# Kernel optimization log

Hardware: AMD Instinct MI355X
Metric: run time of the kernel (lower is better)

## Reference

```python
import jax, jax.numpy as jnp
import numpy as np

N = 50000      # nodes
E = 800000     # edges
IN_DIM = 256
HID = 96
OUT = 64
K = 2
ALPHA = 0.15
SCALING = 1.8  # NormalizedGCNConv scaling_factor
EPS = 1e-12    # torch F.normalize eps


def setup_inputs() -> dict:
    key = jax.random.key(0)
    ks = jax.random.split(key, 8)
    x = jax.random.normal(ks[0], (N, IN_DIM), jnp.float32)
    edge_index = jax.random.randint(ks[1], (2, E), 0, N, dtype=jnp.int64)
    def lin(k, fi, fo):
        s = 1.0 / np.sqrt(fi)
        kw, kb = jax.random.split(k)
        W = jax.random.uniform(kw, (fi, fo), jnp.float32, -s, s)
        b = jax.random.uniform(kb, (fo,), jnp.float32, -s, s)
        return W, b
    W0, b0 = lin(ks[2], IN_DIM, HID)   # convs[0]
    W1, b1 = lin(ks[3], HID, HID)      # convs[1]
    Wx, bx = lin(ks[4], HID, OUT)      # convx
    return {"x": x, "edge_index": edge_index,
            "W0": W0, "b0": b0, "W1": W1, "b1": b1, "Wx": Wx, "bx": bx}


def _l2norm(x):
    n = jnp.linalg.norm(x, axis=1, keepdims=True)
    return x / jnp.maximum(n, EPS)


def _gcn_norm(edge_index):
    # add self loops, symmetric normalization D^-1/2 (A+I) D^-1/2
    loop = jnp.arange(N, dtype=edge_index.dtype)
    row = jnp.concatenate([edge_index[0], loop])
    col = jnp.concatenate([edge_index[1], loop])
    deg = jax.ops.segment_sum(jnp.ones(row.shape[0], jnp.float32), col, num_segments=N)
    dinv = jnp.where(deg > 0, jax.lax.rsqrt(jnp.maximum(deg, 1.0)), 0.0)
    norm = dinv[row] * dinv[col]   # [E+N]
    return row, col, norm


def _norm_gcn_conv(x, W, b, row, col, norm):
    # linear -> L2 normalize * 1.8 -> APPNP(K, alpha), eval mode (no dropout)
    x = x @ W + b
    x = _l2norm(x) * SCALING
    h = x
    for _ in range(K):
        agg = jax.ops.segment_sum(x[row] * norm[:, None], col, num_segments=N)
        x = (1.0 - ALPHA) * agg + ALPHA * h
    return x


def reference(x, edge_index, W0, b0, W1, b1, Wx, bx):
    row, col, norm = _gcn_norm(edge_index)
    out = jax.nn.relu(_norm_gcn_conv(x, W0, b0, row, col, norm))
    # depth=3, link_len=2: loop runs i=1 only, residual condition never fires
    out = _l2norm(_norm_gcn_conv(out, W1, b1, row, col, norm)) * 1.5
    return _norm_gcn_conv(out, Wx, bx, row, col, norm)
```

## Files before the change

kernel.cpp:

```cpp
#include <hip/hip_runtime.h>
#include <hip/hip_fp16.h>
#include <math.h>

#define BETA_C 0.85f
#define ALF_C  0.15f
#define SLOTS 48

typedef _Float16 f16x8 __attribute__((ext_vector_type(8)));
typedef float f32x4 __attribute__((ext_vector_type(4)));

__device__ inline f16x8 as_h8(uint4 v) { union { uint4 u; f16x8 h; } U; U.u = v; return U.h; }

__global__ __launch_bounds__(256) void k_fill_tlp(
        const int* __restrict__ row, const int* __restrict__ col,
        int* __restrict__ cur, int* __restrict__ adj, int E, unsigned mulc) {
    int cls = blockIdx.x & 7;
    int e = (blockIdx.x >> 3) * 256 + threadIdx.x;
    if (e >= E) return;
    int c = col[e];
    if ((int)(((unsigned long long)(unsigned)c * mulc) >> 32) != cls) return;
    int p = atomicAdd(&cur[c], 1);
    if (p < SLOTS) adj[(size_t)c * SLOTS + p] = row[e];
}

__global__ void k_prep(const int* __restrict__ cur, float2* __restrict__ dinv2,
                       int* __restrict__ adj, int n, int t0,
                       const float* __restrict__ W0, const float* __restrict__ W1,
                       const float* __restrict__ Wx, ushort* __restrict__ WT0,
                       ushort* __restrict__ WT1, ushort* __restrict__ WTx) {
    int idx = blockIdx.x * blockDim.x + threadIdx.x;
    if (idx < n) {
        int deg = cur[idx];
        float degf = (float)deg + 1.0f;
        dinv2[idx] = make_float2(rsqrtf(degf), ALF_C * sqrtf(degf));
        int ds = min(deg, SLOTS);
        int d4 = (ds + 3) & ~3;
        int* ap = adj + (size_t)idx * SLOTS;
        for (int p = ds; p < d4; ++p) ap[p] = idx;
    } else if (idx >= t0) {
        const int S0 = 96 * 256, S1 = 96 * 96, S2 = 64 * 96;
        int li = idx - t0;
        const float* W; ushort* WT; int FI, FO;
        if (li < S0)           { W = W0; WT = WT0; FI = 256; FO = 96; }
        else if (li < S0 + S1) { W = W1; WT = WT1; FI = 96;  FO = 96; li -= S0; }
        else if (li < S0+S1+S2){ W = Wx; WT = WTx; FI = 96;  FO = 64; li -= S0 + S1; }
        else return;
        int nrow = li / FI, k = li % FI;
        _Float16 hv = (_Float16)W[(size_t)k * FO + nrow];
        WT[li] = *(ushort*)&hv;
    }
}

template<int FI, int FO, int ASRC_F16>
__global__ __launch_bounds__(256) void k_gemm_mfma(
        const void* __restrict__ Xv, const ushort* __restrict__ WT,
        const float* __restrict__ Bias, const float2* __restrict__ dinv2,
        ushort* __restrict__ H, int n, float scale) {
    constexpr int NT = FO / 16;
    constexpr int CPR = FI / 8;
    __shared__ ushort sA[64 * FI];
    __shared__ ushort sW[FO * FI];
    const int tid = threadIdx.x;
    const int rb = blockIdx.x * 64;

    {
        constexpr int TOT = FO * CPR;
#pragma unroll
        for (int idx = tid; idx < TOT; idx += 256) {
            int nrow = idx / CPR, c = idx % CPR;
            uint4 v = *(((const uint4*)WT) + (size_t)nrow * CPR + c);
            int byte = ((nrow * FI + c * 8) * 2) ^ ((nrow & 7) << 4);
            *(uint4*)((char*)sW + byte) = v;
        }
    }
    {
        constexpr int TOT = 64 * CPR;
#pragma unroll
        for (int idx = tid; idx < TOT; idx += 256) {
            int r = idx / CPR, c = idx % CPR;
            int gr = rb + r;
            uint4 v = make_uint4(0u, 0u, 0u, 0u);
            if (ASRC_F16) {
                if (gr < n) v = *(((const uint4*)Xv) + (size_t)gr * CPR + c);
            } else {
                if (gr < n) {
                    const float4* Xp = (const float4*)Xv;
                    float4 f0 = Xp[(size_t)gr * (FI / 4) + c * 2];
                    float4 f1 = Xp[(size_t)gr * (FI / 4) + c * 2 + 1];
                    _Float16 hv[8] = {(_Float16)f0.x, (_Float16)f0.y, (_Float16)f0.z,
                                      (_Float16)f0.w, (_Float16)f1.x, (_Float16)f1.y,
                                      (_Float16)f1.z, (_Float16)f1.w};
                    v = *(uint4*)hv;
                }
            }
            int byte = ((r * FI + c * 8) * 2) ^ ((r & 7) << 4);
            *(uint4*)((char*)sA + byte) = v;
        }
    }
    __syncthreads();

    const int lane = tid & 63;
    const int wave = tid >> 6;
    const int lcol = lane & 15;
    const int lk = lane >> 4;

    f32x4 acc[NT];
#pragma unroll
    for (int t = 0; t < NT; ++t) acc[t] = (f32x4){0.f, 0.f, 0.f, 0.f};

    const int arow = wave * 16 + lcol;
    char* sAb = (char*)sA;
    char* sWb = (char*)sW;
#pragma unroll
    for (int s = 0; s < FI / 32; ++s) {
        int abyte = ((arow * FI + s * 32 + lk * 8) * 2) ^ ((arow & 7) << 4);
        f16x8 af = *(f16x8*)(sAb + abyte);
#pragma unroll
        for (int t = 0; t < NT; ++t) {
            int nrow = t * 16 + lcol;
            int bbyte = ((nrow * FI + s * 32 + lk * 8) * 2) ^ ((nrow & 7) << 4);
            f16x8 bf = *(f16x8*)(sWb + bbyte);
            acc[t] = __builtin_amdgcn_mfma_f32_16x16x32_f16(af, bf, acc[t], 0, 0, 0);
        }
    }

    float bv[NT];
#pragma unroll
    for (int t = 0; t < NT; ++t) bv[t] = Bias[t * 16 + lcol];
    float ss[4] = {0.f, 0.f, 0.f, 0.f};
#pragma unroll
    for (int t = 0; t < NT; ++t)
#pragma unroll
        for (int r = 0; r < 4; ++r) {
            acc[t][r] += bv[t];
            ss[r] += acc[t][r] * acc[t][r];
        }
    for (int m = 1; m < 16; m <<= 1) {
#pragma unroll
        for (int r = 0; r < 4; ++r) ss[r] += __shfl_xor(ss[r], m, 64);
    }
#pragma unroll
    for (int r = 0; r < 4; ++r) {
        int grow = rb + wave * 16 + lk * 4 + r;
        if (grow < n) {
            float sc = scale * dinv2[grow].x / fmaxf(sqrtf(ss[r]), 1e-12f);
#pragma unroll
            for (int t = 0; t < NT; ++t) {
                _Float16 hv = (_Float16)(acc[t][r] * sc);
                H[(size_t)grow * FO + t * 16 + lcol] = *(ushort*)&hv;
            }
        }
    }
}

__device__ inline void unpack8(uint4 v, float* f) {
    union { uint4 u; _Float16 h[8]; } U; U.u = v;
#pragma unroll
    for (int i = 0; i < 8; ++i) f[i] = (float)U.h[i];
}

template<int C8>
__device__ inline void gather_h(const uint4* __restrict__ tab,
                                const int* __restrict__ ap,
                                int d4, int j, f16x8& A0, f16x8& A1) {
    const int4* ap4 = (const int4*)ap;
    int e = 0;
    for (; e + 8 <= d4; e += 8) {
        int4 a0 = ap4[e >> 2];
        int4 a1 = ap4[(e >> 2) + 1];
        uint4 v0 = tab[(size_t)(unsigned)a0.x * C8 + j];
        uint4 v1 = tab[(size_t)(unsigned)a0.y * C8 + j];
        uint4 v2 = tab[(size_t)(unsigned)a0.z * C8 + j];
        uint4 v3 = tab[(size_t)(unsigned)a0.w * C8 + j];
        uint4 v4 = tab[(size_t)(unsigned)a1.x * C8 + j];
        uint4 v5 = tab[(size_t)(unsigned)a1.y * C8 + j];
        uint4 v6 = tab[(size_t)(unsigned)a1.z * C8 + j];
        uint4 v7 = tab[(size_t)(unsigned)a1.w * C8 + j];
        A0 += (as_h8(v0) + as_h8(v1)) + (as_h8(v2) + as_h8(v3));
        A1 += (as_h8(v4) + as_h8(v5)) + (as_h8(v6) + as_h8(v7));
    }
    if (e < d4) {
        int4 a0 = ap4[e >> 2];
        uint4 v0 = tab[(size_t)(unsigned)a0.x * C8 + j];
        uint4 v1 = tab[(size_t)(unsigned)a0.y * C8 + j];
        uint4 v2 = tab[(size_t)(unsigned)a0.z * C8 + j];
        uint4 v3 = tab[(size_t)(unsigned)a0.w * C8 + j];
        A0 += as_h8(v0) + as_h8(v1);
        A1 += as_h8(v2) + as_h8(v3);
    }
}

template<int C8, int TPB>
__global__ __launch_bounds__(TPB) void k_prop1(
        const uint4* __restrict__ y0, uint4* __restrict__ y1,
        const int* __restrict__ adj, const int* __restrict__ cnt,
        const float2* __restrict__ dinv2, int n) {
    int tid = threadIdx.x;
    int j = tid % C8, cl = tid / C8;
    int c = blockIdx.x * (TPB / C8) + cl;
    if (c >= n) return;
    uint4 sv = y0[(size_t)c * C8 + j];
    float d = dinv2[c].x;
    float a = BETA_C * d * d;
    int deg = min(cnt[c], SLOTS);
    int d4 = (deg + 3) & ~3;
    float coef_s = (a + ALF_C) - a * (float)(d4 - deg);
    f16x8 A0 = {0, 0, 0, 0, 0, 0, 0, 0};
    f16x8 A1 = {0, 0, 0, 0, 0, 0, 0, 0};
    gather_h<C8>(y0, adj + (size_t)c * SLOTS, d4, j, A0, A1);
    float sf[8];
    unpack8(sv, sf);
    _Float16 hv[8];
#pragma unroll
    for (int i = 0; i < 8; ++i) {
        float acc = (float)A0[i] + (float)A1[i];
        hv[i] = (_Float16)(a * acc + coef_s * sf[i]);
    }
    y1[(size_t)c * C8 + j] = *(uint4*)hv;
}

template<int C8, int TPB, int ACT, int OUTF32, int NORM>
__global__ __launch_bounds__(TPB) void k_prop2(
        const uint4* __restrict__ y1, const uint4* __restrict__ y0,
        void* __restrict__ out, const int* __restrict__ adj,
        const int* __restrict__ cnt, const float2* __restrict__ dinv2,
        int n, float nscale) {
    __shared__ float ssh[NORM ? TPB : 1];
    int tid = threadIdx.x;
    int j = tid % C8, cl = tid / C8;
    int c = blockIdx.x * (TPB / C8) + cl;
    if (!NORM && c >= n) return;
    bool on = !NORM || c < n;
    float res[8] = {0, 0, 0, 0, 0, 0, 0, 0};
    if (on) {
        uint4 sv1 = y1[(size_t)c * C8 + j];
        uint4 sv0 = y0[(size_t)c * C8 + j];
        float2 dv = dinv2[c];
        float a = BETA_C * dv.x;
        float t = dv.y;
        int deg = min(cnt[c], SLOTS);
        int d4 = (deg + 3) & ~3;
        float coef_s = a * (1.0f - (float)(d4 - deg));
        f16x8 A0 = {0, 0, 0, 0, 0, 0, 0, 0};
        f16x8 A1 = {0, 0, 0, 0, 0, 0, 0, 0};
        gather_h<C8>(y1, adj + (size_t)c * SLOTS, d4, j, A0, A1);
        float sf[8], tf[8];
        unpack8(sv1, sf);
        unpack8(sv0, tf);
#pragma unroll
        for (int i = 0; i < 8; ++i) {
            float acc = (float)A0[i] + (float)A1[i];
            res[i] = a * acc + coef_s * sf[i] + t * tf[i];
            if (ACT) res[i] = fmaxf(res[i], 0.f);
        }
    }
    if (NORM) {
        float part = 0.f;
#pragma unroll
        for (int i = 0; i < 8; ++i) part += res[i] * res[i];
        ssh[tid] = part;
        __syncthreads();
        if (!on) return;
        float tot = 0.f;
#pragma unroll
        for (int q = 0; q < C8; ++q) tot += ssh[cl * C8 + q];
        float sc = nscale / fmaxf(sqrtf(tot), 1e-12f);
        _Float16 hv[8];
#pragma unroll
        for (int i = 0; i < 8; ++i) hv[i] = (_Float16)(res[i] * sc);
        ((uint4*)out)[(size_t)c * C8 + j] = *(uint4*)hv;
    } else if (OUTF32) {
        float4* op = (float4*)out;
        op[(size_t)c * (C8 * 2) + j * 2]     = make_float4(res[0], res[1], res[2], res[3]);
        op[(size_t)c * (C8 * 2) + j * 2 + 1] = make_float4(res[4], res[5], res[6], res[7]);
    } else {
        _Float16 hv[8];
#pragma unroll
        for (int i = 0; i < 8; ++i) hv[i] = (_Float16)res[i];
        ((uint4*)out)[(size_t)c * C8 + j] = *(uint4*)hv;
    }
}

extern "C" void kernel_launch(void* const* d_in, const int* in_sizes, int n_in,
                              void* d_out, int out_size, void* d_ws, size_t ws_size,
                              hipStream_t stream) {
    const float* x  = (const float*)d_in[0];
    const int*   ei = (const int*)d_in[1];
    const float* W0 = (const float*)d_in[2];
    const float* b0 = (const float*)d_in[3];
    const float* W1 = (const float*)d_in[4];
    const float* b1 = (const float*)d_in[5];
    const float* Wx = (const float*)d_in[6];
    const float* bx = (const float*)d_in[7];
    float* out = (float*)d_out;

    const int N = in_sizes[0] / 256;
    const int E = in_sizes[1] / 2;
    const int* row = ei;
    const int* col = ei + E;

    char* ws = (char*)d_ws;
    size_t off = 0;
    auto alloc = [&](size_t bytes) -> char* {
        char* p = ws + off;
        off += (bytes + 255) & ~(size_t)255;
        return p;
    };
    int*    cur   = (int*)alloc((size_t)N * 4);
    float2* dinv2 = (float2*)alloc((size_t)N * 8);
    int*    adj   = (int*)alloc((size_t)N * SLOTS * 4);
    ushort* WT0   = (ushort*)alloc((size_t)96 * 256 * 2);
    ushort* WT1   = (ushort*)alloc((size_t)96 * 96 * 2);
    ushort* WTx   = (ushort*)alloc((size_t)64 * 96 * 2);
    ushort* Hh    = (ushort*)alloc((size_t)N * 96 * 2);
    ushort* T1h   = (ushort*)alloc((size_t)N * 96 * 2);
    ushort* T2h   = (ushort*)alloc((size_t)N * 96 * 2);
    (void)ws_size; (void)n_in; (void)out_size;

    unsigned mulc = (unsigned)((((unsigned long long)8 << 32) + (unsigned)N - 1) / (unsigned)N);

    hipMemsetAsync(cur, 0, (size_t)N * 4, stream);
    {
        int chunks = (E + 255) / 256;
        k_fill_tlp<<<chunks * 8, 256, 0, stream>>>(row, col, cur, adj, E, mulc);
    }
    {
        int t0 = ((N + 255) / 256) * 256;
        int tot = t0 + 96 * 256 + 96 * 96 + 64 * 96;
        k_prep<<<(tot + 255) / 256, 256, 0, stream>>>(cur, dinv2, adj, N, t0,
                                                      W0, W1, Wx, WT0, WT1, WTx);
    }

    int gblk = (N + 63) / 64;
    int gp12 = (N + 15) / 16;
    int gp8  = (N + 31) / 32;

    k_gemm_mfma<256, 96, 0><<<gblk, 256, 0, stream>>>(x, WT0, b0, dinv2, Hh, N, 1.8f);
    k_prop1<12, 192><<<gp12, 192, 0, stream>>>(
        (const uint4*)Hh, (uint4*)T1h, adj, cur, dinv2, N);
    k_prop2<12, 192, 1, 0, 0><<<gp12, 192, 0, stream>>>(
        (const uint4*)T1h, (const uint4*)Hh, T2h, adj, cur, dinv2, N, 0.f);

    k_gemm_mfma<96, 96, 1><<<gblk, 256, 0, stream>>>(T2h, WT1, b1, dinv2, Hh, N, 1.8f);
    k_prop1<12, 192><<<gp12, 192, 0, stream>>>(
        (const uint4*)Hh, (uint4*)T1h, adj, cur, dinv2, N);
    k_prop2<12, 192, 0, 0, 1><<<gp12, 192, 0, stream>>>(
        (const uint4*)T1h, (const uint4*)Hh, T2h, adj, cur, dinv2, N, 1.5f);

    k_gemm_mfma<96, 64, 1><<<gblk, 256, 0, stream>>>(T2h, WTx, bx, dinv2, Hh, N, 1.8f);
    k_prop1<8, 256><<<gp8, 256, 0, stream>>>(
        (const uint4*)Hh, (uint4*)T1h, adj, cur, dinv2, N);
    k_prop2<8, 256, 0, 1, 0><<<gp8, 256, 0, stream>>>(
        (const uint4*)T1h, (const uint4*)Hh, out, adj, cur, dinv2, N, 0.f);
}
```

Measured before the change: 219.1 us.

## Gather neighbor features from FP8 shadow copies in first two conv layers

The GEMM and prop1 kernels now also write a scaled FP8 copy of their outputs. The first two layers' propagation kernels gather neighbor rows from that FP8 copy instead of FP16, which halves the bytes moved per random gather, and accumulate in fp32. The cost is extra FP8 stores and conversion work, plus lower precision in the aggregated messages that may push accuracy close to tolerance. The adjacency and edge-index loads are also marked nontemporal.

```diff
diff --git a/kernel.cpp b/kernel.cpp
--- a/kernel.cpp
+++ b/kernel.cpp
@@ -5,11 +5,37 @@
 #define BETA_C 0.85f
 #define ALF_C  0.15f
 #define SLOTS 48
+#define SCALE_Q 16.0f
+#define INV_SQ  0.0625f
 
 typedef _Float16 f16x8 __attribute__((ext_vector_type(8)));
 typedef float f32x4 __attribute__((ext_vector_type(4)));
+typedef float f32x2 __attribute__((ext_vector_type(2)));
+typedef int i32x4 __attribute__((ext_vector_type(4)));
 
 __device__ inline f16x8 as_h8(uint4 v) { union { uint4 u; f16x8 h; } U; U.u = v; return U.h; }
+
+__device__ inline void unpack8(uint4 v, float* f) {
+    union { uint4 u; _Float16 h[8]; } U; U.u = v;
+#pragma unroll
+    for (int i = 0; i < 8; ++i) f[i] = (float)U.h[i];
+}
+
+__device__ inline void acc_q(uint2 q, float* acc) {
+    f32x2 f0 = __builtin_amdgcn_cvt_pk_f32_fp8((int)q.x, false);
+    f32x2 f1 = __builtin_amdgcn_cvt_pk_f32_fp8((int)q.x, true);
+    f32x2 f2 = __builtin_amdgcn_cvt_pk_f32_fp8((int)q.y, false);
+    f32x2 f3 = __builtin_amdgcn_cvt_pk_f32_fp8((int)q.y, true);
+    acc[0] += f0.x; acc[1] += f0.y; acc[2] += f1.x; acc[3] += f1.y;
+    acc[4] += f2.x; acc[5] += f2.y; acc[6] += f3.x; acc[7] += f3.y;
+}
+__device__ inline uint2 pack_q(const float* r) {
+    int lo = __builtin_amdgcn_cvt_pk_fp8_f32(r[0] * SCALE_Q, r[1] * SCALE_Q, 0, false);
+    lo = __builtin_amdgcn_cvt_pk_fp8_f32(r[2] * SCALE_Q, r[3] * SCALE_Q, lo, true);
+    int hi = __builtin_amdgcn_cvt_pk_fp8_f32(r[4] * SCALE_Q, r[5] * SCALE_Q, 0, false);
+    hi = __builtin_amdgcn_cvt_pk_fp8_f32(r[6] * SCALE_Q, r[7] * SCALE_Q, hi, true);
+    return make_uint2((unsigned)lo, (unsigned)hi);
+}
 
 __global__ __launch_bounds__(256) void k_fill_tlp(
         const int* __restrict__ row, const int* __restrict__ col,
@@ -17,10 +43,11 @@
     int cls = blockIdx.x & 7;
     int e = (blockIdx.x >> 3) * 256 + threadIdx.x;
     if (e >= E) return;
-    int c = col[e];
+    int c = __builtin_nontemporal_load(col + e);
     if ((int)(((unsigned long long)(unsigned)c * mulc) >> 32) != cls) return;
+    int r = __builtin_nontemporal_load(row + e);
     int p = atomicAdd(&cur[c], 1);
-    if (p < SLOTS) adj[(size_t)c * SLOTS + p] = row[e];
+    if (p < SLOTS) adj[(size_t)c * SLOTS + p] = r;
 }
 
 __global__ void k_prep(const int* __restrict__ cur, float2* __restrict__ dinv2,
@@ -51,11 +78,12 @@
     }
 }
 
-template<int FI, int FO, int ASRC_F16>
+template<int FI, int FO, int ASRC_F16, int WQ>
 __global__ __launch_bounds__(256) void k_gemm_mfma(
         const void* __restrict__ Xv, const ushort* __restrict__ WT,
         const float* __restrict__ Bias, const float2* __restrict__ dinv2,
-        ushort* __restrict__ H, int n, float scale) {
+        ushort* __restrict__ H, unsigned char* __restrict__ Hq,
+        int n, float scale) {
     constexpr int NT = FO / 16;
     constexpr int CPR = FI / 8;
     __shared__ ushort sA[64 * FI];
@@ -146,85 +174,127 @@
             float sc = scale * dinv2[grow].x / fmaxf(sqrtf(ss[r]), 1e-12f);
 #pragma unroll
             for (int t = 0; t < NT; ++t) {
-                _Float16 hv = (_Float16)(acc[t][r] * sc);
+                float v = acc[t][r] * sc;
+                _Float16 hv = (_Float16)v;
                 H[(size_t)grow * FO + t * 16 + lcol] = *(ushort*)&hv;
+                if (WQ) {
+                    float vs = v * SCALE_Q;
+                    int b = __builtin_amdgcn_cvt_pk_fp8_f32(vs, vs, 0, false);
+                    Hq[(size_t)grow * FO + t * 16 + lcol] = (unsigned char)(b & 0xff);
+                }
             }
         }
     }
 }
 
-__device__ inline void unpack8(uint4 v, float* f) {
-    union { uint4 u; _Float16 h[8]; } U; U.u = v;
-#pragma unroll
-    for (int i = 0; i < 8; ++i) f[i] = (float)U.h[i];
+template<int C8>
+__device__ inline void gather_q(const unsigned char* __restrict__ tq,
+                                const int* __restrict__ ap,
+                                int d4, int j, float* acc) {
+    const size_t RB = C8 * 8;
+    const int jb = j * 8;
+    int e = 0;
+    for (; e + 8 <= d4; e += 8) {
+        i32x4 a0 = __builtin_nontemporal_load((const i32x4*)ap + (e >> 2));
+        i32x4 a1 = __builtin_nontemporal_load((const i32x4*)ap + (e >> 2) + 1);
+        uint2 q0 = *(const uint2*)(tq + (size_t)(unsigned)a0[0] * RB + jb);
+        uint2 q1 = *(const uint2*)(tq + (size_t)(unsigned)a0[1] * RB + jb);
+        uint2 q2 = *(const uint2*)(tq + (size_t)(unsigned)a0[2] * RB + jb);
+        uint2 q3 = *(const uint2*)(tq + (size_t)(unsigned)a0[3] * RB + jb);
+        uint2 q4 = *(const uint2*)(tq + (size_t)(unsigned)a1[0] * RB + jb);
+        uint2 q5 = *(const uint2*)(tq + (size_t)(unsigned)a1[1] * RB + jb);
+        uint2 q6 = *(const uint2*)(tq + (size_t)(unsigned)a1[2] * RB + jb);
+        uint2 q7 = *(const uint2*)(tq + (size_t)(unsigned)a1[3] * RB + jb);
+        acc_q(q0, acc); acc_q(q1, acc); acc_q(q2, acc); acc_q(q3, acc);
+        acc_q(q4, acc); acc_q(q5, acc); acc_q(q6, acc); acc_q(q7, acc);
+    }
+    if (e < d4) {
+        i32x4 a0 = __builtin_nontemporal_load((const i32x4*)ap + (e >> 2));
+        uint2 q0 = *(const uint2*)(tq + (size_t)(unsigned)a0[0] * RB + jb);
+        uint2 q1 = *(const uint2*)(tq + (size_t)(unsigned)a0[1] * RB + jb);
+        uint2 q2 = *(const uint2*)(tq + (size_t)(unsigned)a0[2] * RB + jb);
+        uint2 q3 = *(const uint2*)(tq + (size_t)(unsigned)a0[3] * RB + jb);
+        acc_q(q0, acc); acc_q(q1, acc); acc_q(q2, acc); acc_q(q3, acc);
+    }
 }
 
 template<int C8>
 __device__ inline void gather_h(const uint4* __restrict__ tab,
                                 const int* __restrict__ ap,
                                 int d4, int j, f16x8& A0, f16x8& A1) {
-    const int4* ap4 = (const int4*)ap;
     int e = 0;
     for (; e + 8 <= d4; e += 8) {
-        int4 a0 = ap4[e >> 2];
-        int4 a1 = ap4[(e >> 2) + 1];
-        uint4 v0 = tab[(size_t)(unsigned)a0.x * C8 + j];
-        uint4 v1 = tab[(size_t)(unsigned)a0.y * C8 + j];
-        uint4 v2 = tab[(size_t)(unsigned)a0.z * C8 + j];
-        uint4 v3 = tab[(size_t)(unsigned)a0.w * C8 + j];
-        uint4 v4 = tab[(size_t)(unsigned)a1.x * C8 + j];
-        uint4 v5 = tab[(size_t)(unsigned)a1.y * C8 + j];
-        uint4 v6 = tab[(size_t)(unsigned)a1.z * C8 + j];
-        uint4 v7 = tab[(size_t)(unsigned)a1.w * C8 + j];
+        i32x4 a0 = __builtin_nontemporal_load((const i32x4*)ap + (e >> 2));
+        i32x4 a1 = __builtin_nontemporal_load((const i32x4*)ap + (e >> 2) + 1);
+        uint4 v0 = tab[(size_t)(unsigned)a0[0] * C8 + j];
+        uint4 v1 = tab[(size_t)(unsigned)a0[1] * C8 + j];
+        uint4 v2 = tab[(size_t)(unsigned)a0[2] * C8 + j];
+        uint4 v3 = tab[(size_t)(unsigned)a0[3] * C8 + j];
+        uint4 v4 = tab[(size_t)(unsigned)a1[0] * C8 + j];
+        uint4 v5 = tab[(size_t)(unsigned)a1[1] * C8 + j];
+        uint4 v6 = tab[(size_t)(unsigned)a1[2] * C8 + j];
+        uint4 v7 = tab[(size_t)(unsigned)a1[3] * C8 + j];
         A0 += (as_h8(v0) + as_h8(v1)) + (as_h8(v2) + as_h8(v3));
         A1 += (as_h8(v4) + as_h8(v5)) + (as_h8(v6) + as_h8(v7));
     }
     if (e < d4) {
-        int4 a0 = ap4[e >> 2];
-        uint4 v0 = tab[(size_t)(unsigned)a0.x * C8 + j];
-        uint4 v1 = tab[(size_t)(unsigned)a0.y * C8 + j];
-        uint4 v2 = tab[(size_t)(unsigned)a0.z * C8 + j];
-        uint4 v3 = tab[(size_t)(unsigned)a0.w * C8 + j];
+        i32x4 a0 = __builtin_nontemporal_load((const i32x4*)ap + (e >> 2));
+        uint4 v0 = tab[(size_t)(unsigned)a0[0] * C8 + j];
+        uint4 v1 = tab[(size_t)(unsigned)a0[1] * C8 + j];
+        uint4 v2 = tab[(size_t)(unsigned)a0[2] * C8 + j];
+        uint4 v3 = tab[(size_t)(unsigned)a0[3] * C8 + j];
         A0 += as_h8(v0) + as_h8(v1);
         A1 += as_h8(v2) + as_h8(v3);
     }
 }
 
-template<int C8, int TPB>
+template<int C8, int TPB, int QG, int WQ>
 __global__ __launch_bounds__(TPB) void k_prop1(
-        const uint4* __restrict__ y0, uint4* __restrict__ y1,
+        const uint4* __restrict__ y0h, const unsigned char* __restrict__ y0q,
+        uint4* __restrict__ y1h, unsigned char* __restrict__ y1q,
         const int* __restrict__ adj, const int* __restrict__ cnt,
         const float2* __restrict__ dinv2, int n) {
     int tid = threadIdx.x;
     int j = tid % C8, cl = tid / C8;
     int c = blockIdx.x * (TPB / C8) + cl;
     if (c >= n) return;
-    uint4 sv = y0[(size_t)c * C8 + j];
+    uint4 sv = y0h[(size_t)c * C8 + j];
     float d = dinv2[c].x;
     float a = BETA_C * d * d;
     int deg = min(cnt[c], SLOTS);
     int d4 = (deg + 3) & ~3;
     float coef_s = (a + ALF_C) - a * (float)(d4 - deg);
-    f16x8 A0 = {0, 0, 0, 0, 0, 0, 0, 0};
-    f16x8 A1 = {0, 0, 0, 0, 0, 0, 0, 0};
-    gather_h<C8>(y0, adj + (size_t)c * SLOTS, d4, j, A0, A1);
+    float acc[8] = {0, 0, 0, 0, 0, 0, 0, 0};
+    if (QG) {
+        gather_q<C8>(y0q, adj + (size_t)c * SLOTS, d4, j, acc);
+#pragma unroll
+        for (int i = 0; i < 8; ++i) acc[i] *= INV_SQ;
+    } else {
+        f16x8 A0 = {0, 0, 0, 0, 0, 0, 0, 0};
+        f16x8 A1 = {0, 0, 0, 0, 0, 0, 0, 0};
+        gather_h<C8>(y0h, adj + (size_t)c * SLOTS, d4, j, A0, A1);
+#pragma unroll
+        for (int i = 0; i < 8; ++i) acc[i] = (float)A0[i] + (float)A1[i];
+    }
     float sf[8];
     unpack8(sv, sf);
+    float r[8];
     _Float16 hv[8];
 #pragma unroll
     for (int i = 0; i < 8; ++i) {
-        float acc = (float)A0[i] + (float)A1[i];
-        hv[i] = (_Float16)(a * acc + coef_s * sf[i]);
-    }
-    y1[(size_t)c * C8 + j] = *(uint4*)hv;
-}
-
-template<int C8, int TPB, int ACT, int OUTF32, int NORM>
+        r[i] = a * acc[i] + coef_s * sf[i];
+        hv[i] = (_Float16)r[i];
+    }
+    y1h[(size_t)c * C8 + j] = *(uint4*)hv;
+    if (WQ) *(uint2*)(y1q + (size_t)c * (C8 * 8) + j * 8) = pack_q(r);
+}
+
+template<int C8, int TPB, int ACT, int OUTF32, int NORM, int QG>
 __global__ __launch_bounds__(TPB) void k_prop2(
-        const uint4* __restrict__ y1, const uint4* __restrict__ y0,
-        void* __restrict__ out, const int* __restrict__ adj,
-        const int* __restrict__ cnt, const float2* __restrict__ dinv2,
-        int n, float nscale) {
+        const uint4* __restrict__ y1h, const unsigned char* __restrict__ y1q,
+        const uint4* __restrict__ y0h, void* __restrict__ out,
+        const int* __restrict__ adj, const int* __restrict__ cnt,
+        const float2* __restrict__ dinv2, int n, float nscale) {
     __shared__ float ssh[NORM ? TPB : 1];
     int tid = threadIdx.x;
     int j = tid % C8, cl = tid / C8;
@@ -233,24 +303,32 @@
     bool on = !NORM || c < n;
     float res[8] = {0, 0, 0, 0, 0, 0, 0, 0};
     if (on) {
-        uint4 sv1 = y1[(size_t)c * C8 + j];
-        uint4 sv0 = y0[(size_t)c * C8 + j];
+        uint4 sv1 = y1h[(size_t)c * C8 + j];
+        uint4 sv0 = y0h[(size_t)c * C8 + j];
         float2 dv = dinv2[c];
         float a = BETA_C * dv.x;
         float t = dv.y;
         int deg = min(cnt[c], SLOTS);
         int d4 = (deg + 3) & ~3;
         float coef_s = a * (1.0f - (float)(d4 - deg));
-        f16x8 A0 = {0, 0, 0, 0, 0, 0, 0, 0};
-        f16x8 A1 = {0, 0, 0, 0, 0, 0, 0, 0};
-        gather_h<C8>(y1, adj + (size_t)c * SLOTS, d4, j, A0, A1);
+        float acc[8] = {0, 0, 0, 0, 0, 0, 0, 0};
+        if (QG) {
+            gather_q<C8>(y1q, adj + (size_t)c * SLOTS, d4, j, acc);
+#pragma unroll
+            for (int i = 0; i < 8; ++i) acc[i] *= INV_SQ;
+        } else {
+            f16x8 A0 = {0, 0, 0, 0, 0, 0, 0, 0};
+            f16x8 A1 = {0, 0, 0, 0, 0, 0, 0, 0};
+            gather_h<C8>(y1h, adj + (size_t)c * SLOTS, d4, j, A0, A1);
+#pragma unroll
+            for (int i = 0; i < 8; ++i) acc[i] = (float)A0[i] + (float)A1[i];
+        }
         float sf[8], tf[8];
         unpack8(sv1, sf);
         unpack8(sv0, tf);
 #pragma unroll
         for (int i = 0; i < 8; ++i) {
-            float acc = (float)A0[i] + (float)A1[i];
-            res[i] = a * acc + coef_s * sf[i] + t * tf[i];
+            res[i] = a * acc[i] + coef_s * sf[i] + t * tf[i];
             if (ACT) res[i] = fmaxf(res[i], 0.f);
         }
     }
@@ -315,6 +393,8 @@
     ushort* Hh    = (ushort*)alloc((size_t)N * 96 * 2);
     ushort* T1h   = (ushort*)alloc((size_t)N * 96 * 2);
     ushort* T2h   = (ushort*)alloc((size_t)N * 96 * 2);
+    unsigned char* Hq  = (unsigned char*)alloc((size_t)N * 96);
+    unsigned char* T1q = (unsigned char*)alloc((size_t)N * 96);
     (void)ws_size; (void)n_in; (void)out_size;
 
     unsigned mulc = (unsigned)((((unsigned long long)8 << 32) + (unsigned)N - 1) / (unsigned)N);
@@ -335,21 +415,21 @@
     int gp12 = (N + 15) / 16;
     int gp8  = (N + 31) / 32;
 
-    k_gemm_mfma<256, 96, 0><<<gblk, 256, 0, stream>>>(x, WT0, b0, dinv2, Hh, N, 1.8f);
-    k_prop1<12, 192><<<gp12, 192, 0, stream>>>(
-        (const uint4*)Hh, (uint4*)T1h, adj, cur, dinv2, N);
-    k_prop2<12, 192, 1, 0, 0><<<gp12, 192, 0, stream>>>(
-        (const uint4*)T1h, (const uint4*)Hh, T2h, adj, cur, dinv2, N, 0.f);
-
-    k_gemm_mfma<96, 96, 1><<<gblk, 256, 0, stream>>>(T2h, WT1, b1, dinv2, Hh, N, 1.8f);
-    k_prop1<12, 192><<<gp12, 192, 0, stream>>>(
-        (const uint4*)Hh, (uint4*)T1h, adj, cur, dinv2, N);
-    k_prop2<12, 192, 0, 0, 1><<<gp12, 192, 0, stream>>>(
-        (const uint4*)T1h, (const uint4*)Hh, T2h, adj, cur, dinv2, N, 1.5f);
-
-    k_gemm_mfma<96, 64, 1><<<gblk, 256, 0, stream>>>(T2h, WTx, bx, dinv2, Hh, N, 1.8f);
-    k_prop1<8, 256><<<gp8, 256, 0, stream>>>(
-        (const uint4*)Hh, (uint4*)T1h, adj, cur, dinv2, N);
-    k_prop2<8, 256, 0, 1, 0><<<gp8, 256, 0, stream>>>(
-        (const uint4*)T1h, (const uint4*)Hh, out, adj, cur, dinv2, N, 0.f);
-}
+    k_gemm_mfma<256, 96, 0, 1><<<gblk, 256, 0, stream>>>(x, WT0, b0, dinv2, Hh, Hq, N, 1.8f);
+    k_prop1<12, 192, 1, 1><<<gp12, 192, 0, stream>>>(
+        (const uint4*)Hh, Hq, (uint4*)T1h, T1q, adj, cur, dinv2, N);
+    k_prop2<12, 192, 1, 0, 0, 1><<<gp12, 192, 0, stream>>>(
+        (const uint4*)T1h, T1q, (const uint4*)Hh, T2h, adj, cur, dinv2, N, 0.f);
+
+    k_gemm_mfma<96, 96, 1, 1><<<gblk, 256, 0, stream>>>(T2h, WT1, b1, dinv2, Hh, Hq, N, 1.8f);
+    k_prop1<12, 192, 1, 1><<<gp12, 192, 0, stream>>>(
+        (const uint4*)Hh, Hq, (uint4*)T1h, T1q, adj, cur, dinv2, N);
+    k_prop2<12, 192, 0, 0, 1, 1><<<gp12, 192, 0, stream>>>(
+        (const uint4*)T1h, T1q, (const uint4*)Hh, T2h, adj, cur, dinv2, N, 1.5f);
+
+    k_gemm_mfma<96, 64, 1, 0><<<gblk, 256, 0, stream>>>(T2h, WTx, bx, dinv2, Hh, Hq, N, 1.8f);
+    k_prop1<8, 256, 0, 0><<<gp8, 256, 0, stream>>>(
+        (const uint4*)Hh, Hq, (uint4*)T1h, T1q, adj, cur, dinv2, N);
+    k_prop2<8, 256, 0, 1, 0, 0><<<gp8, 256, 0, stream>>>(
+        (const uint4*)T1h, T1q, (const uint4*)Hh, out, adj, cur, dinv2, N, 0.f);
+}
```

Result: no change. 216.0 us (median of 2 runs) (-1.4%).
